# Kernel tuning notes

Measured on AMD Instinct MI355X. Metric: run time of the kernel, lower is better.

The kernel has to match this reference:

```python
import jax, jax.numpy as jnp
import numpy as np

NQ = 9  # 9 qubits per 3x3 patch; state shape (M, 2,...,2), axis (NQ-q) holds qubit q (qiskit little-endian)

def _ax(q):
    return NQ - q

def _bcast(theta):
    theta = jnp.asarray(theta)
    if theta.ndim == 1:  # per-patch angle -> broadcast over 8 remaining qubit axes
        return theta.reshape((-1,) + (1,) * (NQ - 1))
    return theta

def apply_1q(state, q, m00, m01, m10, m11):
    ax = _ax(q)
    s0 = jnp.take(state, 0, axis=ax)
    s1 = jnp.take(state, 1, axis=ax)
    return jnp.stack([m00 * s0 + m01 * s1, m10 * s0 + m11 * s1], axis=ax)

def apply_ry(state, q, theta):
    th = _bcast(theta) * 0.5
    c = jnp.cos(th).astype(state.dtype)
    s = jnp.sin(th).astype(state.dtype)
    return apply_1q(state, q, c, -s, s, c)

def apply_rz(state, q, theta):
    th = _bcast(theta) * 0.5
    e = jnp.exp(-1j * th.astype(jnp.complex64))
    return apply_1q(state, q, e, 0.0, 0.0, jnp.conj(e))

def apply_cx(state, c, t):
    axc, axt = _ax(c), _ax(t)
    sc0 = jnp.take(state, 0, axis=axc)
    sc1 = jnp.take(state, 1, axis=axc)
    axt2 = axt - 1 if axt > axc else axt
    sc1 = jnp.flip(sc1, axis=axt2)  # X on target within control=1 subspace
    return jnp.stack([sc0, sc1], axis=axc)

def apply_crx(state, c, t, theta):
    axc, axt = _ax(c), _ax(t)
    sc0 = jnp.take(state, 0, axis=axc)
    sc1 = jnp.take(state, 1, axis=axc)
    axt2 = axt - 1 if axt > axc else axt
    t0 = jnp.take(sc1, 0, axis=axt2)
    t1 = jnp.take(sc1, 1, axis=axt2)
    co = jnp.cos(theta * 0.5)
    si = jnp.sin(theta * 0.5)
    sc1 = jnp.stack([co * t0 - 1j * si * t1, -1j * si * t0 + co * t1], axis=axt2)
    return jnp.stack([sc0, sc1], axis=axc)

def qcnn_batched(angles, w):
    """angles: (M, 9) input rotation angles. w: (42,) shared weights. Returns (M, 3) = [<X>,<Y>,<Z>] on qubit 0."""
    M = angles.shape[0]
    state = jnp.zeros((M,) + (2,) * NQ, dtype=jnp.complex64)
    state = state.at[(slice(None),) + (0,) * NQ].set(1.0)
    for q in range(NQ):  # input encoding
        state = apply_ry(state, q, angles[:, q])
    wi = 0
    # conv1: RY + RZ on all 9 qubits, ring CNOT
    for q in range(NQ):
        state = apply_ry(state, q, w[wi]); wi += 1
    for q in range(NQ):
        state = apply_rz(state, q, w[wi]); wi += 1
    for i in range(NQ):
        state = apply_cx(state, i, (i + 1) % NQ)
    # pool1: 6 CRX gates
    for (c, t) in [(1, 0), (2, 0), (4, 3), (5, 3), (7, 6), (8, 6)]:
        state = apply_crx(state, c, t, w[wi]); wi += 1
    # conv2 on qubits [0,3,6]
    for q in [0, 3, 6]:
        state = apply_ry(state, q, w[wi]); wi += 1
    for q in [0, 3, 6]:
        state = apply_rz(state, q, w[wi]); wi += 1
    for (c, t) in [(0, 3), (3, 6), (6, 0)]:
        state = apply_cx(state, c, t)
    state = apply_ry(state, 0, w[wi])
    state = apply_rz(state, 3, w[wi + 1]); wi += 2
    # pool2
    state = apply_crx(state, 3, 0, w[wi])
    state = apply_crx(state, 3, 6, w[wi + 1])
    state = apply_ry(state, 0, w[wi + 2])
    state = apply_ry(state, 6, w[wi + 3]); wi += 4
    # conv3
    state = apply_ry(state, 0, w[wi])
    state = apply_ry(state, 6, w[wi + 1])
    state = apply_cx(state, 0, 6)
    state = apply_rz(state, 0, w[wi + 2])
    state = apply_rz(state, 6, w[wi + 3]); wi += 4
    # pool3
    state = apply_crx(state, 6, 0, w[wi])
    state = apply_ry(state, 0, w[wi + 1]); wi += 2
    assert wi == 42
    # expectations <X>,<Y>,<Z> on qubit 0 (last axis)
    a0 = jnp.take(state, 0, axis=NQ)
    a1 = jnp.take(state, 1, axis=NQ)
    axes = tuple(range(1, NQ))
    z = jnp.sum(jnp.conj(a0) * a1, axis=axes)
    ex = 2.0 * jnp.real(z)
    ey = 2.0 * jnp.imag(z)
    ez = jnp.sum(jnp.abs(a0) ** 2 - jnp.abs(a1) ** 2, axis=axes)
    return jnp.stack([ex, ey, ez], axis=-1).astype(jnp.float32)

def setup_inputs() -> dict:
    key = jax.random.key(0)
    k1, k2, k3 = jax.random.split(key, 3)
    B, H, WS, NCLS = 8, 28, 3, 10
    n = H - WS + 1  # 26 patches per side
    x = jax.random.uniform(k1, (B, 1, H, H), dtype=jnp.float32)
    w = jax.random.normal(k2, (42,), dtype=jnp.float32)
    fc_w = jax.random.normal(k3, (NCLS, n * n * 3), dtype=jnp.float32) * 0.02
    fc_b = jnp.zeros((NCLS,), dtype=jnp.float32)
    return {"x": x, "w": w, "fc_w": fc_w, "fc_b": fc_b}

def reference(x, w, fc_w, fc_b):
    B, H, WS = x.shape[0], x.shape[2], 3
    n = H - WS + 1
    # extract 3x3 patches, row-major within window (matches torch unfold+view)
    patches = jnp.stack([x[:, 0, i:i + n, j:j + n] for i in range(WS) for j in range(WS)], axis=-1)  # (B,n,n,9)
    angles = patches.reshape(B * n * n, WS * WS) * jnp.pi
    bloch = qcnn_batched(angles, w)  # (B*N, 3)
    feats = bloch.reshape(B, n * n * 3)  # patch-major [X,Y,Z] per patch, matches torch.cat over patches
    return feats @ fc_w.T + fc_b
```

## Files before the change

kernel.cpp:

```cpp
#include <hip/hip_runtime.h>


__device__ __forceinline__ float shx(float v, int m) { return __shfl_xor(v, m, 64); }
__device__ __forceinline__ float fsel(int c, float a, float b) { return c ? a : b; }

template <int TM> __device__ __forceinline__
void ry_r(float (&re)[8], float (&im)[8], float c, float s) {
#pragma unroll
  for (int r0 = 0; r0 < 8; ++r0) if (!(r0 & TM)) {
    const int r1 = r0 | TM;
    float a = re[r0], bb = re[r1];
    re[r0] = c * a - s * bb; re[r1] = s * a + c * bb;
    a = im[r0]; bb = im[r1];
    im[r0] = c * a - s * bb; im[r1] = s * a + c * bb;
  }
}

template <int TM> __device__ __forceinline__
void rz_r(float (&re)[8], float (&im)[8], float c, float s) {
#pragma unroll
  for (int r = 0; r < 8; ++r) {
    const float sg = (r & TM) ? s : -s;
    const float a = re[r], bb = im[r];
    re[r] = c * a - sg * bb;
    im[r] = c * bb + sg * a;
  }
}

template <int CM, int TM> __device__ __forceinline__
void cx_rr(float (&re)[8], float (&im)[8]) {
#pragma unroll
  for (int r0 = 0; r0 < 8; ++r0) if ((r0 & CM) && !(r0 & TM)) {
    const int r1 = r0 | TM;
    float t = re[r0]; re[r0] = re[r1]; re[r1] = t;
    t = im[r0]; im[r0] = im[r1]; im[r1] = t;
  }
}

template <int CL, int TM> __device__ __forceinline__
void cx_lr(float (&re)[8], float (&im)[8], int lane) {
  const bool ctl = (lane & CL) != 0;
#pragma unroll
  for (int r0 = 0; r0 < 8; ++r0) if (!(r0 & TM)) {
    const int r1 = r0 | TM;
    float a0 = re[r0], a1 = re[r1];
    re[r0] = ctl ? a1 : a0; re[r1] = ctl ? a0 : a1;
    a0 = im[r0]; a1 = im[r1];
    im[r0] = ctl ? a1 : a0; im[r1] = ctl ? a0 : a1;
  }
}

template <int CM, int TL> __device__ __forceinline__
void cx_rl(float (&re)[8], float (&im)[8]) {
#pragma unroll
  for (int r = 0; r < 8; ++r) if (r & CM) {
    re[r] = shx(re[r], TL);
    im[r] = shx(im[r], TL);
  }
}

template <int CL, int TL> __device__ __forceinline__
void cx_ll(float (&re)[8], float (&im)[8], int lane) {
  const bool ctl = (lane & CL) != 0;
#pragma unroll
  for (int r = 0; r < 8; ++r) {
    const float orr = shx(re[r], TL), oii = shx(im[r], TL);
    re[r] = ctl ? orr : re[r];
    im[r] = ctl ? oii : im[r];
  }
}

template <int CM, int TM> __device__ __forceinline__
void crx_rr(float (&re)[8], float (&im)[8], float co, float si) {
#pragma unroll
  for (int r0 = 0; r0 < 8; ++r0) if ((r0 & CM) && !(r0 & TM)) {
    const int r1 = r0 | TM;
    const float r0r = re[r0], r0i = im[r0], r1r = re[r1], r1i = im[r1];
    re[r0] = co * r0r + si * r1i; im[r0] = co * r0i - si * r1r;
    re[r1] = co * r1r + si * r0i; im[r1] = co * r1i - si * r0r;
  }
}

template <int TM> __device__ __forceinline__
void rx_l(float (&re)[8], float (&im)[8], float c, float s) {
#pragma unroll
  for (int r0 = 0; r0 < 8; ++r0) if (!(r0 & TM)) {
    const int r1 = r0 | TM;
    const float r0r = re[r0], r0i = im[r0], r1r = re[r1], r1i = im[r1];
    re[r0] = c * r0r + s * r1i;  im[r0] = c * r0i - s * r1r;
    re[r1] = c * r1r + s * r0i;  im[r1] = c * r1i - s * r0r;
  }
}

__global__ __launch_bounds__(256) void qcnn_fused(const float* __restrict__ x,
                                                  const float* __restrict__ w,
                                                  float* __restrict__ feats) {
  __shared__ float  wenc[9];
  __shared__ float  wrzl[6];
  __shared__ float2 rztab[8];
  __shared__ float2 g[24];
  __shared__ float2 rxtab[3][4];
  __shared__ float2 Msh[8][8];

  const int tid = threadIdx.x;
  if (tid < 9) {
    wenc[tid] = w[tid];
  } else if (tid < 15) {
    const int qmap[6] = {1, 2, 4, 5, 7, 8};
    wrzl[tid - 9] = 0.5f * w[9 + qmap[tid - 9]];
  } else if (tid >= 16 && tid < 24) {
    const int r = tid - 16;
    const float ph = ((r & 1) ? 0.5f : -0.5f) * w[9]
                   + ((r & 2) ? 0.5f : -0.5f) * w[12]
                   + ((r & 4) ? 0.5f : -0.5f) * w[15];
    float s, c; __sincosf(ph, &s, &c);
    rztab[r] = make_float2(c, s);
  } else if (tid >= 24 && tid < 48) {
    float s, c; __sincosf(0.5f * w[18 + tid - 24], &s, &c);
    g[tid - 24] = make_float2(c, s);
  } else if (tid >= 48 && tid < 60) {
    const int k = tid - 48, a = k >> 2, cb = k & 3;
    float th = 0.0f;
    if (cb & 1) th += w[18 + 2 * a];
    if (cb & 2) th += w[19 + 2 * a];
    float s, c; __sincosf(0.5f * th, &s, &c);
    rxtab[a][cb] = make_float2(c, s);
  }
  __syncthreads();

  if (tid < 8) {
    float re[8], im[8];
#pragma unroll
    for (int r = 0; r < 8; ++r) { re[r] = (r == tid) ? 1.0f : 0.0f; im[r] = 0.0f; }
    ry_r<1>(re, im, g[6].x, g[6].y);
    ry_r<2>(re, im, g[7].x, g[7].y);
    ry_r<4>(re, im, g[8].x, g[8].y);
    rz_r<1>(re, im, g[9].x, g[9].y);
    rz_r<2>(re, im, g[10].x, g[10].y);
    rz_r<4>(re, im, g[11].x, g[11].y);
    cx_rr<1, 2>(re, im);
    cx_rr<2, 4>(re, im);
    cx_rr<4, 1>(re, im);
    ry_r<1>(re, im, g[12].x, g[12].y);
    rz_r<2>(re, im, g[13].x, g[13].y);
    crx_rr<2, 1>(re, im, g[14].x, g[14].y);
    crx_rr<2, 4>(re, im, g[15].x, g[15].y);
    ry_r<1>(re, im, g[16].x, g[16].y);
    ry_r<4>(re, im, g[17].x, g[17].y);
    ry_r<1>(re, im, g[18].x, g[18].y);
    ry_r<4>(re, im, g[19].x, g[19].y);
    cx_rr<1, 4>(re, im);
    rz_r<1>(re, im, g[20].x, g[20].y);
    rz_r<4>(re, im, g[21].x, g[21].y);
    crx_rr<4, 1>(re, im, g[22].x, g[22].y);
    ry_r<1>(re, im, g[23].x, g[23].y);
#pragma unroll
    for (int i = 0; i < 8; ++i) Msh[i][tid] = make_float2(re[i], im[i]);
  }
  __syncthreads();

  const int lane = tid & 63;
  const unsigned p = blockIdx.x * 4u + (tid >> 6);
  const unsigned b = p / 676u;
  const unsigned rem = p - b * 676u;
  const unsigned i = rem / 26u, j = rem - i * 26u;
  const float* xb = x + b * 784u;

  float c_enc = 0.0f, s_enc = 0.0f;
  if (lane < 9) {
    const int di = lane / 3, dj = lane - di * 3;
    const float ang = fmaf(xb[(i + di) * 28u + (j + dj)],
                           3.14159265358979323846f, wenc[lane]) * 0.5f;
    __sincosf(ang, &s_enc, &c_enc);
  }
  float cq[9], sq[9];
#pragma unroll
  for (int q = 0; q < 9; ++q) { cq[q] = __shfl(c_enc, q, 64); sq[q] = __shfl(s_enc, q, 64); }

  float F = fsel(lane & 1,  sq[1], cq[1]);
  F      *= fsel(lane & 2,  sq[2], cq[2]);
  F      *= fsel(lane & 4,  sq[4], cq[4]);
  F      *= fsel(lane & 8,  sq[5], cq[5]);
  F      *= fsel(lane & 16, sq[7], cq[7]);
  F      *= fsel(lane & 32, sq[8], cq[8]);
  const float ph = (lane & 1  ? wrzl[0] : -wrzl[0])
                 + (lane & 2  ? wrzl[1] : -wrzl[1])
                 + (lane & 4  ? wrzl[2] : -wrzl[2])
                 + (lane & 8  ? wrzl[3] : -wrzl[3])
                 + (lane & 16 ? wrzl[4] : -wrzl[4])
                 + (lane & 32 ? wrzl[5] : -wrzl[5]);
  float sl, cl; __sincosf(ph, &sl, &cl);

  float re[8], im[8];
#pragma unroll
  for (int r = 0; r < 8; ++r) {
    const float pr = (r & 1 ? sq[0] : cq[0]) * (r & 2 ? sq[3] : cq[3]) * (r & 4 ? sq[6] : cq[6]);
    const float A = F * pr;
    const float cr = rztab[r].x, sr = rztab[r].y;
    const float cc = cl * cr - sl * sr;
    const float ss = sl * cr + cl * sr;
    re[r] = A * cc;
    im[r] = A * ss;
  }

  cx_rl<1, 1>(re, im);
  cx_ll<1, 2>(re, im, lane);
  cx_lr<2, 2>(re, im, lane);
  cx_rl<2, 4>(re, im);
  cx_ll<4, 8>(re, im, lane);
  cx_lr<8, 4>(re, im, lane);
  cx_rl<4, 16>(re, im);
  cx_ll<16, 32>(re, im, lane);
  cx_lr<32, 1>(re, im, lane);

  const float2 x0 = rxtab[0][lane & 3];
  const float2 x1 = rxtab[1][(lane >> 2) & 3];
  const float2 x2 = rxtab[2][(lane >> 4) & 3];
  rx_l<1>(re, im, x0.x, x0.y);
  rx_l<2>(re, im, x1.x, x1.y);
  rx_l<4>(re, im, x2.x, x2.y);

  float nre[8], nim[8];
#pragma unroll
  for (int oi = 0; oi < 8; ++oi) {
    float ar = 0.0f, ai = 0.0f;
#pragma unroll
    for (int jj = 0; jj < 8; ++jj) {
      const float2 m = Msh[oi][jj];
      ar = fmaf(m.x, re[jj], ar);  ar = fmaf(-m.y, im[jj], ar);
      ai = fmaf(m.x, im[jj], ai);  ai = fmaf(m.y, re[jj], ai);
    }
    nre[oi] = ar; nim[oi] = ai;
  }

  float zr = 0.f, zi = 0.f, pe = 0.f;
#pragma unroll
  for (int r0 = 0; r0 < 8; r0 += 2) {
    const int r1 = r0 + 1;
    zr += nre[r0] * nre[r1] + nim[r0] * nim[r1];
    zi += nre[r0] * nim[r1] - nim[r0] * nre[r1];
    pe += nre[r0] * nre[r0] + nim[r0] * nim[r0];
  }
#pragma unroll
  for (int m = 1; m < 64; m <<= 1) { zr += shx(zr, m); zi += shx(zi, m); pe += shx(pe, m); }

  if (lane == 0) {
    feats[p * 3u + 0u] = 2.0f * zr;
    feats[p * 3u + 1u] = 2.0f * zi;
    feats[p * 3u + 2u] = 2.0f * pe - 1.0f;
  }
}

__global__ __launch_bounds__(256) void fc_kernel(const float* __restrict__ feats,
                                                 const float* __restrict__ fc_w,
                                                 const float* __restrict__ fc_b,
                                                 float* __restrict__ out) {
  const int b = blockIdx.x / 10, c = blockIdx.x - b * 10;
  const float* f = feats + b * 2028;
  const float* wr = fc_w + c * 2028;
  float acc = 0.0f;
  for (int k = threadIdx.x; k < 2028; k += 256) acc += f[k] * wr[k];
#pragma unroll
  for (int m = 1; m < 64; m <<= 1) acc += __shfl_xor(acc, m, 64);
  __shared__ float sbuf[4];
  const int lane = threadIdx.x & 63, wv = threadIdx.x >> 6;
  if (lane == 0) sbuf[wv] = acc;
  __syncthreads();
  if (threadIdx.x == 0) out[b * 10 + c] = sbuf[0] + sbuf[1] + sbuf[2] + sbuf[3] + fc_b[c];
}

extern "C" void kernel_launch(void* const* d_in, const int* in_sizes, int n_in,
                              void* d_out, int out_size, void* d_ws, size_t ws_size,
                              hipStream_t stream) {
  const float* x    = (const float*)d_in[0];
  const float* w    = (const float*)d_in[1];
  const float* fc_w = (const float*)d_in[2];
  const float* fc_b = (const float*)d_in[3];
  float* out = (float*)d_out;

  const int B = in_sizes[0] / 784;
  const int npatch = B * 676;

  float* feats = (float*)d_ws;

  qcnn_fused<<<npatch / 4, 256, 0, stream>>>(x, w, feats);
  fc_kernel<<<B * 10, 256, 0, stream>>>(feats, fc_w, fc_b, out);
}
```

Before: 75.59 us.

## Factor post-CNOT-ring state into tensor products, removing lane shuffles

Uses the fact that the encoded state is a product state with diagonal RZ phases and the CNOT ring is a basis permutation. Each lane's amplitudes are built directly as products of per-qubit complex factors in the permuted basis, which replaces the nine shuffle-based CNOT stages and the separate RX passes. The 8x8 matrix in shared memory is now read as float4, and the second barrier is moved after the state build so table setup overlaps with per-lane work. The cost is a more intricate index algebra that must exactly match the gate order.

```diff
diff --git a/kernel.cpp b/kernel.cpp
--- a/kernel.cpp
+++ b/kernel.cpp
@@ -2,7 +2,10 @@
 
 
 __device__ __forceinline__ float shx(float v, int m) { return __shfl_xor(v, m, 64); }
-__device__ __forceinline__ float fsel(int c, float a, float b) { return c ? a : b; }
+
+__device__ __forceinline__ float2 cmul(float2 a, float2 b) {
+  return make_float2(a.x * b.x - a.y * b.y, a.x * b.y + a.y * b.x);
+}
 
 template <int TM> __device__ __forceinline__
 void ry_r(float (&re)[8], float (&im)[8], float c, float s) {
@@ -15,7 +18,6 @@
     im[r0] = c * a - s * bb; im[r1] = s * a + c * bb;
   }
 }
-
 template <int TM> __device__ __forceinline__
 void rz_r(float (&re)[8], float (&im)[8], float c, float s) {
 #pragma unroll
@@ -26,7 +28,6 @@
     im[r] = c * bb + sg * a;
   }
 }
-
 template <int CM, int TM> __device__ __forceinline__
 void cx_rr(float (&re)[8], float (&im)[8]) {
 #pragma unroll
@@ -36,40 +37,6 @@
     t = im[r0]; im[r0] = im[r1]; im[r1] = t;
   }
 }
-
-template <int CL, int TM> __device__ __forceinline__
-void cx_lr(float (&re)[8], float (&im)[8], int lane) {
-  const bool ctl = (lane & CL) != 0;
-#pragma unroll
-  for (int r0 = 0; r0 < 8; ++r0) if (!(r0 & TM)) {
-    const int r1 = r0 | TM;
-    float a0 = re[r0], a1 = re[r1];
-    re[r0] = ctl ? a1 : a0; re[r1] = ctl ? a0 : a1;
-    a0 = im[r0]; a1 = im[r1];
-    im[r0] = ctl ? a1 : a0; im[r1] = ctl ? a0 : a1;
-  }
-}
-
-template <int CM, int TL> __device__ __forceinline__
-void cx_rl(float (&re)[8], float (&im)[8]) {
-#pragma unroll
-  for (int r = 0; r < 8; ++r) if (r & CM) {
-    re[r] = shx(re[r], TL);
-    im[r] = shx(im[r], TL);
-  }
-}
-
-template <int CL, int TL> __device__ __forceinline__
-void cx_ll(float (&re)[8], float (&im)[8], int lane) {
-  const bool ctl = (lane & CL) != 0;
-#pragma unroll
-  for (int r = 0; r < 8; ++r) {
-    const float orr = shx(re[r], TL), oii = shx(im[r], TL);
-    re[r] = ctl ? orr : re[r];
-    im[r] = ctl ? oii : im[r];
-  }
-}
-
 template <int CM, int TM> __device__ __forceinline__
 void crx_rr(float (&re)[8], float (&im)[8], float co, float si) {
 #pragma unroll
@@ -81,45 +48,26 @@
   }
 }
 
-template <int TM> __device__ __forceinline__
-void rx_l(float (&re)[8], float (&im)[8], float c, float s) {
-#pragma unroll
-  for (int r0 = 0; r0 < 8; ++r0) if (!(r0 & TM)) {
-    const int r1 = r0 | TM;
-    const float r0r = re[r0], r0i = im[r0], r1r = re[r1], r1i = im[r1];
-    re[r0] = c * r0r + s * r1i;  im[r0] = c * r0i - s * r1r;
-    re[r1] = c * r1r + s * r0i;  im[r1] = c * r1i - s * r0r;
-  }
-}
-
 __global__ __launch_bounds__(256) void qcnn_fused(const float* __restrict__ x,
                                                   const float* __restrict__ w,
                                                   float* __restrict__ feats) {
   __shared__ float  wenc[9];
-  __shared__ float  wrzl[6];
-  __shared__ float2 rztab[8];
+  __shared__ float2 zcs[9];
   __shared__ float2 g[24];
   __shared__ float2 rxtab[3][4];
-  __shared__ float2 Msh[8][8];
+  __shared__ float4 Msh[8][4];
 
   const int tid = threadIdx.x;
   if (tid < 9) {
     wenc[tid] = w[tid];
-  } else if (tid < 15) {
-    const int qmap[6] = {1, 2, 4, 5, 7, 8};
-    wrzl[tid - 9] = 0.5f * w[9 + qmap[tid - 9]];
-  } else if (tid >= 16 && tid < 24) {
-    const int r = tid - 16;
-    const float ph = ((r & 1) ? 0.5f : -0.5f) * w[9]
-                   + ((r & 2) ? 0.5f : -0.5f) * w[12]
-                   + ((r & 4) ? 0.5f : -0.5f) * w[15];
-    float s, c; __sincosf(ph, &s, &c);
-    rztab[r] = make_float2(c, s);
-  } else if (tid >= 24 && tid < 48) {
-    float s, c; __sincosf(0.5f * w[18 + tid - 24], &s, &c);
-    g[tid - 24] = make_float2(c, s);
-  } else if (tid >= 48 && tid < 60) {
-    const int k = tid - 48, a = k >> 2, cb = k & 3;
+  } else if (tid >= 16 && tid < 25) {
+    float s, c; __sincosf(0.5f * w[9 + (tid - 16)], &s, &c);
+    zcs[tid - 16] = make_float2(c, s);
+  } else if (tid >= 32 && tid < 56) {
+    float s, c; __sincosf(0.5f * w[18 + (tid - 32)], &s, &c);
+    g[tid - 32] = make_float2(c, s);
+  } else if (tid >= 56 && tid < 68) {
+    const int k = tid - 56, a = k >> 2, cb = k & 3;
     float th = 0.0f;
     if (cb & 1) th += w[18 + 2 * a];
     if (cb & 2) th += w[19 + 2 * a];
@@ -154,81 +102,93 @@
     rz_r<4>(re, im, g[21].x, g[21].y);
     crx_rr<4, 1>(re, im, g[22].x, g[22].y);
     ry_r<1>(re, im, g[23].x, g[23].y);
-#pragma unroll
-    for (int i = 0; i < 8; ++i) Msh[i][tid] = make_float2(re[i], im[i]);
-  }
-  __syncthreads();
+    float* mp = (float*)&Msh[0][0];
+#pragma unroll
+    for (int i = 0; i < 8; ++i) {
+      mp[i * 16 + (tid >> 1) * 4 + 2 * (tid & 1) + 0] = re[i];
+      mp[i * 16 + (tid >> 1) * 4 + 2 * (tid & 1) + 1] = im[i];
+    }
+  }
 
   const int lane = tid & 63;
   const unsigned p = blockIdx.x * 4u + (tid >> 6);
   const unsigned b = p / 676u;
   const unsigned rem = p - b * 676u;
   const unsigned i = rem / 26u, j = rem - i * 26u;
-  const float* xb = x + b * 784u;
 
   float c_enc = 0.0f, s_enc = 0.0f;
   if (lane < 9) {
     const int di = lane / 3, dj = lane - di * 3;
-    const float ang = fmaf(xb[(i + di) * 28u + (j + dj)],
-                           3.14159265358979323846f, wenc[lane]) * 0.5f;
+    const float xv = x[b * 784u + (i + di) * 28u + (j + dj)];
+    const float ang = fmaf(xv, 3.14159265358979323846f, wenc[lane]) * 0.5f;
     __sincosf(ang, &s_enc, &c_enc);
   }
-  float cq[9], sq[9];
-#pragma unroll
-  for (int q = 0; q < 9; ++q) { cq[q] = __shfl(c_enc, q, 64); sq[q] = __shfl(s_enc, q, 64); }
-
-  float F = fsel(lane & 1,  sq[1], cq[1]);
-  F      *= fsel(lane & 2,  sq[2], cq[2]);
-  F      *= fsel(lane & 4,  sq[4], cq[4]);
-  F      *= fsel(lane & 8,  sq[5], cq[5]);
-  F      *= fsel(lane & 16, sq[7], cq[7]);
-  F      *= fsel(lane & 32, sq[8], cq[8]);
-  const float ph = (lane & 1  ? wrzl[0] : -wrzl[0])
-                 + (lane & 2  ? wrzl[1] : -wrzl[1])
-                 + (lane & 4  ? wrzl[2] : -wrzl[2])
-                 + (lane & 8  ? wrzl[3] : -wrzl[3])
-                 + (lane & 16 ? wrzl[4] : -wrzl[4])
-                 + (lane & 32 ? wrzl[5] : -wrzl[5]);
-  float sl, cl; __sincosf(ph, &sl, &cl);
-
-  float re[8], im[8];
-#pragma unroll
-  for (int r = 0; r < 8; ++r) {
-    const float pr = (r & 1 ? sq[0] : cq[0]) * (r & 2 ? sq[3] : cq[3]) * (r & 4 ? sq[6] : cq[6]);
-    const float A = F * pr;
-    const float cr = rztab[r].x, sr = rztab[r].y;
-    const float cc = cl * cr - sl * sr;
-    const float ss = sl * cr + cl * sr;
-    re[r] = A * cc;
-    im[r] = A * ss;
-  }
-
-  cx_rl<1, 1>(re, im);
-  cx_ll<1, 2>(re, im, lane);
-  cx_lr<2, 2>(re, im, lane);
-  cx_rl<2, 4>(re, im);
-  cx_ll<4, 8>(re, im, lane);
-  cx_lr<8, 4>(re, im, lane);
-  cx_rl<4, 16>(re, im);
-  cx_ll<16, 32>(re, im, lane);
-  cx_lr<32, 1>(re, im, lane);
-
-  const float2 x0 = rxtab[0][lane & 3];
-  const float2 x1 = rxtab[1][(lane >> 2) & 3];
-  const float2 x2 = rxtab[2][(lane >> 4) & 3];
-  rx_l<1>(re, im, x0.x, x0.y);
-  rx_l<2>(re, im, x1.x, x1.y);
-  rx_l<4>(re, im, x2.x, x2.y);
+  float cqv[9], sqv[9];
+#pragma unroll
+  for (int q = 0; q < 9; ++q) { cqv[q] = __shfl(c_enc, q, 64); sqv[q] = __shfl(s_enc, q, 64); }
+
+  const int l0 = lane & 1, l1 = (lane >> 1) & 1, l2 = (lane >> 2) & 1;
+  const int l3 = (lane >> 3) & 1, l4 = (lane >> 4) & 1, l5 = (lane >> 5) & 1;
+
+  auto tau = [&](int bit, int q) -> float2 {
+    const float2 z = zcs[q];
+    const float m  = bit ? sqv[q] : cqv[q];
+    const float zy = bit ? z.y : -z.y;
+    return make_float2(m * z.x, m * zy);
+  };
+
+  const int a0 = l5, a1 = l0 ^ l5;
+  float2 p00 = cmul(tau(a0, 0), tau(a1, 1));
+  float2 p01 = cmul(tau(a0 ^ 1, 0), tau(a1 ^ 1, 1));
+  float2 p10 = cmul(tau(l1, 3), tau(l2, 4));
+  float2 p11 = cmul(tau(l1 ^ 1, 3), tau(l2 ^ 1, 4));
+  float2 p20 = cmul(tau(l3, 6), tau(l4, 7));
+  float2 p21 = cmul(tau(l3 ^ 1, 6), tau(l4 ^ 1, 7));
+  const float2 T = cmul(cmul(tau(l0 ^ l1, 2), tau(l2 ^ l3, 5)), tau(l4 ^ l5, 8));
+  p20 = cmul(p20, T);
+  p21 = cmul(p21, T);
+
+  {
+    const float2 x0 = rxtab[0][lane & 3];
+    const float2 x1 = rxtab[1][(lane >> 2) & 3];
+    const float2 x2 = rxtab[2][(lane >> 4) & 3];
+    float2 nA, nB;
+    nA = make_float2(x0.x * p00.x + x0.y * p01.y, x0.x * p00.y - x0.y * p01.x);
+    nB = make_float2(x0.x * p01.x + x0.y * p00.y, x0.x * p01.y - x0.y * p00.x);
+    p00 = nA; p01 = nB;
+    nA = make_float2(x1.x * p10.x + x1.y * p11.y, x1.x * p10.y - x1.y * p11.x);
+    nB = make_float2(x1.x * p11.x + x1.y * p10.y, x1.x * p11.y - x1.y * p10.x);
+    p10 = nA; p11 = nB;
+    nA = make_float2(x2.x * p20.x + x2.y * p21.y, x2.x * p20.y - x2.y * p21.x);
+    nB = make_float2(x2.x * p21.x + x2.y * p20.y, x2.x * p21.y - x2.y * p20.x);
+    p20 = nA; p21 = nB;
+  }
+
+  float ure[8], uim[8];
+  {
+    const float2 q00 = cmul(p00, p10), q01v = cmul(p01, p10);
+    const float2 q10 = cmul(p00, p11), q11v = cmul(p01, p11);
+    const float2 qq[4] = {q00, q01v, q10, q11v};
+#pragma unroll
+    for (int r = 0; r < 8; ++r) {
+      const float2 u = cmul(qq[r & 3], (r & 4) ? p21 : p20);
+      ure[r] = u.x; uim[r] = u.y;
+    }
+  }
+
+  __syncthreads();
 
   float nre[8], nim[8];
 #pragma unroll
   for (int oi = 0; oi < 8; ++oi) {
     float ar = 0.0f, ai = 0.0f;
 #pragma unroll
-    for (int jj = 0; jj < 8; ++jj) {
-      const float2 m = Msh[oi][jj];
-      ar = fmaf(m.x, re[jj], ar);  ar = fmaf(-m.y, im[jj], ar);
-      ai = fmaf(m.x, im[jj], ai);  ai = fmaf(m.y, re[jj], ai);
+    for (int jj = 0; jj < 4; ++jj) {
+      const float4 m = Msh[oi][jj];
+      ar = fmaf(m.x, ure[2 * jj], ar);     ar = fmaf(-m.y, uim[2 * jj], ar);
+      ai = fmaf(m.x, uim[2 * jj], ai);     ai = fmaf(m.y, ure[2 * jj], ai);
+      ar = fmaf(m.z, ure[2 * jj + 1], ar); ar = fmaf(-m.w, uim[2 * jj + 1], ar);
+      ai = fmaf(m.z, uim[2 * jj + 1], ai); ai = fmaf(m.w, ure[2 * jj + 1], ai);
     }
     nre[oi] = ar; nim[oi] = ai;
   }
```

After: 70.50 us. -6.7%, faster.
